# Kernel optimization log

Hardware: AMD Instinct MI355X
Metric: run time of the kernel (lower is better)

The kernel has to match this reference:

```python
import jax, jax.numpy as jnp
import numpy as np


def _register_translation(target_images, src_images, upsample_factor):
    # squeeze channel dim -> (B, H, W), promote to complex for FFT
    tgt = target_images[..., 0].astype(jnp.complex64)
    src = src_images[..., 0].astype(jnp.complex64)
    B, H, W = tgt.shape

    target_freq = jnp.fft.fft2(tgt)
    src_freq = jnp.fft.fft2(src)
    # cross-power spectrum (skimage register_translation convention)
    image_product = src_freq * jnp.conj(target_freq)
    cross_corr = jnp.fft.ifft2(image_product)

    # coarse (integer-pixel) peak
    abs_cc = jnp.abs(cross_corr).reshape(B, -1)
    idx = jnp.argmax(abs_cc, axis=1)
    maxima = jnp.stack([idx // W, idx % W], axis=1).astype(jnp.float32)  # (B,2)
    shape_f = jnp.array([H, W], jnp.float32)
    midpoints = jnp.array([H // 2, W // 2], jnp.float32)  # fix(axis_size/2)
    shifts = jnp.where(maxima > midpoints, maxima - shape_f, maxima)

    if upsample_factor > 1:
        uf = float(upsample_factor)
        shifts = jnp.round(shifts * uf) / uf
        region = int(np.ceil(upsample_factor * 1.5))  # upsampled region size
        dftshift = float(np.fix(region / 2.0))
        offsets = dftshift - shifts * uf  # (B,2) sample region offsets

        r_idx = jnp.arange(region, dtype=jnp.float32)
        freq_r = (jnp.fft.fftfreq(H) * H).astype(jnp.float32)  # ifftshift(arange(H)-H//2)
        freq_c = (jnp.fft.fftfreq(W) * W).astype(jnp.float32)
        two_pi = 2.0 * np.pi

        # per-batch small DFT kernels: row (B, region, H), col (B, W, region)
        row_ang = (two_pi / (H * uf)) * (r_idx[None, :, None] - offsets[:, 0][:, None, None]) * freq_r[None, None, :]
        col_ang = (two_pi / (W * uf)) * freq_c[None, :, None] * (r_idx[None, None, :] - offsets[:, 1][:, None, None])
        row_k = jnp.exp(-1j * row_ang)
        col_k = jnp.exp(-1j * col_ang)

        # upsampled DFT of conj(image_product), then conjugate back
        cc_up = jnp.conj(jnp.einsum('brh,bhw,bwc->brc', row_k, jnp.conj(image_product), col_k))
        abs_up = jnp.abs(cc_up).reshape(B, -1)
        idx2 = jnp.argmax(abs_up, axis=1)
        max2 = jnp.stack([idx2 // region, idx2 % region], axis=1).astype(jnp.float32) - dftshift
        shifts = shifts + max2 / uf

    return shifts  # (B, 2) -- (row_shift, col_shift)


def setup_inputs() -> dict:
    key = jax.random.key(0)
    k1, k2 = jax.random.split(key)
    B, H, W = 32, 512, 512
    target_images = jax.random.normal(k1, (B, H, W, 1), dtype=jnp.float32)
    src_images = jax.random.normal(k2, (B, H, W, 1), dtype=jnp.float32)
    return {"target_images": target_images, "src_images": src_images, "upsample_factor": 20}


def reference(target_images, src_images, upsample_factor):
    return _register_translation(target_images, src_images, upsample_factor)
```

## Files before the change

kernel.cpp:

```cpp
#include <hip/hip_runtime.h>
#include <math.h>

#define BN 32
#define HN 512
#define WN 512
#define REGION 30
#define RPAD 32
#define UFV 20.0f
#define DFTSHIFT 15.0f
#define TWO_PI 6.2831853071795864769f
#define HS 8
#define HCH (HN / HS)
#define WS 4

typedef float2 cplx;

__device__ __forceinline__ cplx cmul(cplx a, cplx b){
    return make_float2(a.x*b.x - a.y*b.y, a.x*b.y + a.y*b.x);
}
__device__ __forceinline__ cplx cadd(cplx a, cplx b){
    return make_float2(a.x + b.x, a.y + b.y);
}
__device__ __forceinline__ cplx csub(cplx a, cplx b){
    return make_float2(a.x - b.x, a.y - b.y);
}
__device__ __forceinline__ int brev6(int i){ return (int)(__brev((unsigned)i) >> 26); }
__device__ __forceinline__ int csl(int h, int c){ return c * 546 + h + (h >> 4); }

#define BFLY(a,b,w){ cplx t_ = cmul(w,b); b = make_float2(a.x - t_.x, a.y - t_.y); a = cadd(a, t_); }
#define BFLY1(a,b){ cplx t_ = b; b = make_float2(a.x - t_.x, a.y - t_.y); a = cadd(a, t_); }

__device__ __forceinline__ void fft512_regs(cplx* v, const float2* tw, cplx* ds, int lane){
    const cplx wI  = *(const cplx*)&tw[128];
    const cplx w8a = *(const cplx*)&tw[64];
    const cplx w8b = *(const cplx*)&tw[192];
    BFLY1(v[0],v[1]); BFLY1(v[2],v[3]); BFLY1(v[4],v[5]); BFLY1(v[6],v[7]);
    BFLY1(v[0],v[2]); BFLY(v[1],v[3],wI); BFLY1(v[4],v[6]); BFLY(v[5],v[7],wI);
    BFLY1(v[0],v[4]); BFLY(v[1],v[5],w8a); BFLY(v[2],v[6],wI); BFLY(v[3],v[7],w8b);
    const int h = lane >> 3, lo = lane & 7;
    const int bw = 9 * lane;
    const int br = 72 * h + lo;
    #pragma unroll
    for (int j = 0; j < 8; ++j) ds[bw + j] = v[j];
    asm volatile("s_waitcnt lgkmcnt(0)" ::: "memory");
    #pragma unroll
    for (int j = 0; j < 8; ++j) v[j] = ds[br + 9*j];
    {
        cplx wA = *(const cplx*)&tw[lo<<5];
        BFLY(v[0],v[1],wA); BFLY(v[2],v[3],wA); BFLY(v[4],v[5],wA); BFLY(v[6],v[7],wA);
        cplx wB0 = *(const cplx*)&tw[lo<<4], wB1 = *(const cplx*)&tw[128+(lo<<4)];
        BFLY(v[0],v[2],wB0); BFLY(v[1],v[3],wB1); BFLY(v[4],v[6],wB0); BFLY(v[5],v[7],wB1);
        cplx wC0 = *(const cplx*)&tw[lo<<3], wC1 = *(const cplx*)&tw[64+(lo<<3)];
        cplx wC2 = *(const cplx*)&tw[128+(lo<<3)], wC3 = *(const cplx*)&tw[192+(lo<<3)];
        BFLY(v[0],v[4],wC0); BFLY(v[1],v[5],wC1); BFLY(v[2],v[6],wC2); BFLY(v[3],v[7],wC3);
    }
    #pragma unroll
    for (int j = 0; j < 8; ++j) ds[br + 9*j] = v[j];
    asm volatile("s_waitcnt lgkmcnt(0)" ::: "memory");
    const int br3 = lane + (lane >> 3);
    #pragma unroll
    for (int j = 0; j < 8; ++j) v[j] = ds[br3 + 72*j];
    {
        cplx wD = *(const cplx*)&tw[lane<<2];
        BFLY(v[0],v[1],wD); BFLY(v[2],v[3],wD); BFLY(v[4],v[5],wD); BFLY(v[6],v[7],wD);
        cplx wE0 = *(const cplx*)&tw[lane<<1], wE1 = *(const cplx*)&tw[128+(lane<<1)];
        BFLY(v[0],v[2],wE0); BFLY(v[1],v[3],wE1); BFLY(v[4],v[6],wE0); BFLY(v[5],v[7],wE1);
        cplx wF0 = *(const cplx*)&tw[lane], wF1 = *(const cplx*)&tw[64+lane];
        cplx wF2 = *(const cplx*)&tw[128+lane], wF3 = *(const cplx*)&tw[192+lane];
        BFLY(v[0],v[4],wF0); BFLY(v[1],v[5],wF1); BFLY(v[2],v[6],wF2); BFLY(v[3],v[7],wF3);
    }
}

__global__ void __launch_bounds__(256) row_fft_pack(const float* __restrict__ tgt,
                                                    const float* __restrict__ src,
                                                    cplx* __restrict__ Fz){
    __shared__ float2 tw[256];
    __shared__ cplx ds[4 * 576];
    const int tid = threadIdx.x;
    { float sv, cv; sincosf(-TWO_PI * (float)tid * (1.0f/512.0f), &sv, &cv);
      tw[tid] = make_float2(cv, sv); }
    __syncthreads();
    const int wave = tid >> 6, lane = tid & 63;
    const int rid = blockIdx.x * 4 + wave;
    const float* tr = tgt + (size_t)rid * WN;
    const float* sr = src + (size_t)rid * WN;
    const int rb6 = brev6(lane);
    const int B3[8] = {0,256,128,384,64,320,192,448};
    cplx v[8];
    #pragma unroll
    for (int j = 0; j < 8; ++j){ int o = B3[j] + rb6; v[j] = make_float2(tr[o], sr[o]); }
    fft512_regs(v, (const float2*)tw, ds + wave * 576, lane);
    cplx* orow = Fz + (size_t)rid * WN;
    #pragma unroll
    for (int j = 0; j < 8; ++j) orow[64*j + lane] = v[j];
}

__device__ __forceinline__ void col_fft8(cplx* sm, const float2* tw, int tid){
    const cplx wI  = tw[128];
    const cplx w8a = tw[64];
    const cplx w8b = tw[192];
    const int c  = tid & 7;
    const int k0 = tid >> 3, k1 = k0 + 32;
    const int B3[8] = {0,256,128,384,64,320,192,448};
    cplx ya[8], yb[8];
    {
        const int r0 = brev6(k0), r1 = brev6(k1);
        #pragma unroll
        for (int m = 0; m < 8; ++m){
            ya[m] = sm[csl(B3[m] + r0, c)];
            yb[m] = sm[csl(B3[m] + r1, c)];
        }
    }
    __syncthreads();
    #define P0(x) \
        BFLY1(x[0],x[1]); BFLY1(x[2],x[3]); BFLY1(x[4],x[5]); BFLY1(x[6],x[7]); \
        BFLY1(x[0],x[2]); BFLY(x[1],x[3],wI); BFLY1(x[4],x[6]); BFLY(x[5],x[7],wI); \
        BFLY1(x[0],x[4]); BFLY(x[1],x[5],w8a); BFLY(x[2],x[6],wI); BFLY(x[3],x[7],w8b);
    P0(ya); P0(yb);
    #undef P0
    #pragma unroll
    for (int m = 0; m < 8; ++m){
        sm[csl(8*k0 + m, c)] = ya[m];
        sm[csl(8*k1 + m, c)] = yb[m];
    }
    __syncthreads();
    #pragma unroll
    for (int pass = 1; pass < 3; ++pass){
        const int st = 3*pass + 1;
        const int h1 = 1 << (st - 1);
        #pragma unroll
        for (int gi = 0; gi < 2; ++gi){
            const int k = (tid >> 3) + 32*gi;
            const int q = k & (h1 - 1);
            const int i0 = ((k >> (st - 1)) << (st + 2)) + q;
            cplx x[8];
            #pragma unroll
            for (int m = 0; m < 8; ++m) x[m] = sm[csl(i0 + m*h1, c)];
            cplx w1 = tw[q << (9 - st)];
            BFLY(x[0],x[1],w1); BFLY(x[2],x[3],w1); BFLY(x[4],x[5],w1); BFLY(x[6],x[7],w1);
            cplx w2a = tw[q << (8 - st)];
            cplx w2b = tw[(q << (8 - st)) + 128];
            BFLY(x[0],x[2],w2a); BFLY(x[1],x[3],w2b); BFLY(x[4],x[6],w2a); BFLY(x[5],x[7],w2b);
            cplx w30 = tw[q << (7 - st)];
            cplx w31 = tw[(q << (7 - st)) + 64];
            cplx w32 = tw[(q << (7 - st)) + 128];
            cplx w33 = tw[(q << (7 - st)) + 192];
            BFLY(x[0],x[4],w30); BFLY(x[1],x[5],w31); BFLY(x[2],x[6],w32); BFLY(x[3],x[7],w33);
            #pragma unroll
            for (int m = 0; m < 8; ++m) sm[csl(i0 + m*h1, c)] = x[m];
        }
        __syncthreads();
    }
}

__global__ void col_fft_fwd(cplx* __restrict__ buf){
    const int b  = blockIdx.y;
    const int w0 = blockIdx.x * 8;
    const int tid = threadIdx.x;
    __shared__ cplx sm[4368];
    __shared__ float2 tw[256];
    { float sv, cv; sincosf(-TWO_PI * (float)tid * (1.0f/512.0f), &sv, &cv);
      tw[tid] = make_float2(cv, sv); }
    cplx* base = buf + (size_t)b * HN * WN + w0;
    for (int idx = tid; idx < HN * 4; idx += 256){
        int h = idx >> 2, c2 = (idx & 3) << 1;
        float4 v = *(const float4*)(base + (size_t)h * WN + c2);
        sm[csl(h, c2)]     = make_float2(v.x, v.y);
        sm[csl(h, c2 + 1)] = make_float2(v.z, v.w);
    }
    __syncthreads();
    col_fft8(sm, (const float2*)tw, tid);
    for (int idx = tid; idx < HN * 4; idx += 256){
        int h = idx >> 2, c2 = (idx & 3) << 1;
        cplx a = sm[csl(h, c2)], d = sm[csl(h, c2 + 1)];
        *(float4*)(base + (size_t)h * WN + c2) = make_float4(a.x, a.y, d.x, d.y);
    }
}

__global__ void __launch_bounds__(256) cross_rowinv(cplx* __restrict__ Fz, cplx* __restrict__ cc){
    __shared__ float2 tw[256];
    __shared__ cplx ds[4 * 1184];
    const int tid = threadIdx.x;
    { float sv, cv; sincosf(TWO_PI * (float)tid * (1.0f/512.0f), &sv, &cv);
      tw[tid] = make_float2(cv, sv); }
    __syncthreads();
    const int wave = tid >> 6, lane = tid & 63;
    const int p = blockIdx.x * 4 + wave;
    if (p > 256) return;
    const int b = blockIdx.y;
    const int h1 = p, h2 = (HN - p) & (HN - 1);
    cplx* r1 = Fz + ((size_t)b * HN + h1) * WN;
    cplx* r2 = Fz + ((size_t)b * HN + h2) * WN;
    cplx* A = ds + wave * 1184;
    cplx* B = A + 592;
    #pragma unroll
    for (int u = 0; u < 8; ++u){
        A[lane + 64*u] = r1[lane + 64*u];
        B[lane + 64*u] = r2[lane + 64*u];
    }
    asm volatile("s_waitcnt lgkmcnt(0)" ::: "memory");
    const int rb6 = brev6(lane);
    const int B3[8] = {0,256,128,384,64,320,192,448};
    cplx v1[8];
    #pragma unroll
    for (int j = 0; j < 8; ++j){
        int w  = B3[j] + rb6;
        int wm = (WN - w) & (WN - 1);
        cplx Aw = A[w], Bw = B[w], Am = A[wm], Bm = B[wm];
        { cplx Bc = make_float2(Bm.x, -Bm.y);
          cplx s = cadd(Aw, Bc);
          cplx d = make_float2(Aw.x - Bc.x, Aw.y - Bc.y);
          cplx D = make_float2(d.x*s.x + d.y*s.y, d.y*s.x - d.x*s.y);
          v1[j] = make_float2(0.25f * D.y, -0.25f * D.x); }
        { cplx Ac = make_float2(Am.x, -Am.y);
          cplx s = cadd(Bw, Ac);
          cplx d = make_float2(Bw.x - Ac.x, Bw.y - Ac.y);
          cplx D = make_float2(d.x*s.x + d.y*s.y, d.y*s.x - d.x*s.y);
          r2[w] = make_float2(0.25f * D.y, -0.25f * D.x); }
        r1[w] = v1[j];
    }
    fft512_regs(v1, (const float2*)tw, A, lane);
    cplx* c1 = cc + ((size_t)b * HN + h1) * WN;
    #pragma unroll
    for (int j = 0; j < 8; ++j) c1[64*j + lane] = v1[j];
}

__global__ void colinv_argmax(const cplx* __restrict__ buf, float2* __restrict__ cand){
    const int b  = blockIdx.y;
    const int w0 = blockIdx.x * 8;
    const int tid = threadIdx.x;
    __shared__ cplx sm[4368];
    __shared__ float2 tw[256];
    { float sv, cv; sincosf(TWO_PI * (float)tid * (1.0f/512.0f), &sv, &cv);
      tw[tid] = make_float2(cv, sv); }
    const cplx* base = buf + (size_t)b * HN * WN + w0;
    for (int idx = tid; idx < 257 * 4; idx += 256){
        int h = idx >> 2, c2 = (idx & 3) << 1;
        float4 v = *(const float4*)(base + (size_t)h * WN + c2);
        sm[csl(h, c2)]     = make_float2(v.x, v.y);
        sm[csl(h, c2 + 1)] = make_float2(v.z, v.w);
    }
    __syncthreads();
    for (int idx = tid; idx < 255 * 8; idx += 256){
        int h = 257 + (idx >> 3), c = idx & 7;
        cplx v = sm[csl(HN - h, c)];
        sm[csl(h, c)] = make_float2(v.x, -v.y);
    }
    __syncthreads();
    col_fft8(sm, (const float2*)tw, tid);
    float best = -1.0f; int bidx = 0x7fffffff;
    for (int idx = tid; idx < HN * 8; idx += 256){
        int h = idx >> 3, c = idx & 7;
        cplx v = sm[csl(h, c)];
        float mm = v.x * v.x + v.y * v.y;
        if (mm > best){ best = mm; bidx = h * WN + w0 + c; }
    }
    __shared__ float vals[256];
    __shared__ int   idxs[256];
    vals[tid] = best; idxs[tid] = bidx;
    __syncthreads();
    for (int s = 128; s > 0; s >>= 1){
        if (tid < s){
            if (vals[tid + s] > vals[tid] ||
                (vals[tid + s] == vals[tid] && idxs[tid + s] < idxs[tid])){
                vals[tid] = vals[tid + s]; idxs[tid] = idxs[tid + s];
            }
        }
        __syncthreads();
    }
    if (tid == 0) cand[b * 64 + blockIdx.x] = make_float2(vals[0], __int_as_float(idxs[0]));
}

__global__ void coarse_reduce(const float2* __restrict__ cand, float* __restrict__ small){
    const int b = blockIdx.x, t = threadIdx.x;
    float2 c = cand[b * 64 + t];
    float v = c.x; int ix = __float_as_int(c.y);
    for (int off = 32; off > 0; off >>= 1){
        float v2 = __shfl_down(v, off);
        int   i2 = __shfl_down(ix, off);
        if (v2 > v || (v2 == v && i2 < ix)){ v = v2; ix = i2; }
    }
    if (t == 0){
        int row = ix / WN, col = ix % WN;
        float sr = (row > HN / 2) ? (float)(row - HN) : (float)row;
        float sc = (col > WN / 2) ? (float)(col - WN) : (float)col;
        small[b * 4 + 0] = sr;
        small[b * 4 + 1] = sc;
        small[b * 4 + 2] = DFTSHIFT - sr * UFV;
        small[b * 4 + 3] = DFTSHIFT - sc * UFV;
    }
}

__global__ void __launch_bounds__(256, 3) upsample_T(const cplx* __restrict__ P,
                                                     const float* __restrict__ small,
                                                     cplx* __restrict__ Tpart){
    const int b = blockIdx.y, hs = blockIdx.z;
    const int tid = threadIdx.x;
    const int wp = tid & 31;
    const int rbase = tid >> 5;
    const int w = blockIdx.x * 64 + wp * 2;
    const int h0 = hs * HCH;
    const float off0 = small[b * 4 + 2];
    const float CC = TWO_PI / (HN * UFV);
    __shared__ float2 rk[RPAD][HCH];
    for (int idx = tid; idx < RPAD * HCH; idx += 256){
        int r = idx >> 6, hh = idx & (HCH - 1);
        int h = h0 + hh;
        float fr = (h < HN / 2) ? (float)h : (float)(h - HN);
        float sv, cv; sincosf(-CC * ((float)r - off0) * fr, &sv, &cv);
        rk[r][hh] = make_float2(cv, sv);
    }
    __syncthreads();
    cplx a0[4], a1[4];
    #pragma unroll
    for (int u = 0; u < 4; ++u){ a0[u] = make_float2(0.f,0.f); a1[u] = make_float2(0.f,0.f); }
    const cplx* pc = P + ((size_t)b * HN + h0) * WN + w;

    float4 pvA[4], pvB[4];
    #pragma unroll
    for (int k = 0; k < 4; ++k) pvA[k] = *(const float4*)(pc + (size_t)k * WN);

    #pragma unroll 1
    for (int hh = 0; hh < HCH; hh += 8){
        #pragma unroll
        for (int k = 0; k < 4; ++k)
            pvB[k] = *(const float4*)(pc + (size_t)(hh + 4 + k) * WN);
        #pragma unroll
        for (int k = 0; k < 4; ++k){
            #pragma unroll
            for (int u = 0; u < 4; ++u){
                cplx wv = rk[rbase * 4 + u][hh + k];
                a0[u].x += wv.x * pvA[k].x + wv.y * pvA[k].y;
                a0[u].y += wv.y * pvA[k].x - wv.x * pvA[k].y;
                a1[u].x += wv.x * pvA[k].z + wv.y * pvA[k].w;
                a1[u].y += wv.y * pvA[k].z - wv.x * pvA[k].w;
            }
        }
        if (hh + 8 < HCH){
            #pragma unroll
            for (int k = 0; k < 4; ++k)
                pvA[k] = *(const float4*)(pc + (size_t)(hh + 8 + k) * WN);
        }
        #pragma unroll
        for (int k = 0; k < 4; ++k){
            #pragma unroll
            for (int u = 0; u < 4; ++u){
                cplx wv = rk[rbase * 4 + u][hh + 4 + k];
                a0[u].x += wv.x * pvB[k].x + wv.y * pvB[k].y;
                a0[u].y += wv.y * pvB[k].x - wv.x * pvB[k].y;
                a1[u].x += wv.x * pvB[k].z + wv.y * pvB[k].w;
                a1[u].y += wv.y * pvB[k].z - wv.x * pvB[k].w;
            }
        }
    }

    #pragma unroll
    for (int u = 0; u < 4; ++u){
        int r = rbase * 4 + u;
        if (r < REGION){
            float4* dst = (float4*)(Tpart + (((size_t)hs * BN + b) * REGION + r) * WN + w);
            *dst = make_float4(a0[u].x, a0[u].y, a1[u].x, a1[u].y);
        }
    }
}

__global__ void upsample_U_part(const cplx* __restrict__ Tpart, const cplx* __restrict__ P,
                                const float* __restrict__ small, cplx* __restrict__ Upart){
    const int ws = blockIdx.x, b = blockIdx.y;
    const int tid = threadIdx.x;
    const int w0 = ws * 64;
    const float off0 = small[b * 4 + 2];
    const float off1 = small[b * 4 + 3];
    const float CW = TWO_PI / (WN * UFV);
    const float CH = TWO_PI / (HN * UFV);
    __shared__ float2 Ts[REGION][64];
    __shared__ float2 ck[64][REGION];
    __shared__ float2 p256[64];
    __shared__ float2 T256s[REGION];
    const size_t TS = (size_t)BN * REGION * WN;
    for (int idx = tid; idx < REGION * 64; idx += 256){
        int r = idx >> 6, ww = idx & 63;
        cplx s = make_float2(0.f, 0.f);
        #pragma unroll
        for (int hs = 0; hs < HS; ++hs)
            s = cadd(s, Tpart[(size_t)hs * TS + ((size_t)b * REGION + r) * WN + w0 + ww]);
        Ts[r][ww] = s;
    }
    if (tid < 64) p256[tid] = P[((size_t)b * HN + 256) * WN + w0 + tid];
    if (ws == 0 && tid >= 64 && tid < 64 + REGION){
        int r = tid - 64;
        cplx s = make_float2(0.f, 0.f);
        #pragma unroll
        for (int hs = 0; hs < HS; ++hs)
            s = cadd(s, Tpart[(size_t)hs * TS + ((size_t)b * REGION + r) * WN + 256]);
        T256s[r] = s;
    }
    for (int idx = tid; idx < 64 * REGION; idx += 256){
        int ww = idx / REGION, c = idx - ww * REGION;
        int w = w0 + ww;
        float sv, cv; sincosf(-CW * (float)w * ((float)c - off1), &sv, &cv);
        ck[ww][c] = make_float2(cv, sv);
    }
    __syncthreads();
    const int start = (ws == 0) ? 1 : 0;
    #pragma unroll
    for (int q = 0; q < 4; ++q){
        int o = tid + 256 * q;
        if (o < REGION * REGION){
            int r = o / REGION, c = o - r * REGION;
            float racc = 0.f;
            cplx s2 = make_float2(0.f, 0.f);
            for (int ww = start; ww < 64; ++ww){
                float2 T = Ts[r][ww], K = ck[ww][c];
                racc += T.x * K.x - T.y * K.y;
                float2 pv = p256[ww];
                s2.x += pv.x * K.x + pv.y * K.y;
                s2.y += pv.y * K.x - pv.x * K.y;
            }
            float th = CH * ((float)r - off0) * 256.0f;
            float snt = sinf(th);
            cplx contrib = make_float2(2.f * racc - 2.f * snt * s2.y,
                                       2.f * snt * s2.x);
            if (ws == 0){
                contrib = cadd(contrib, Ts[r][0]);
                float s256, c256; sincosf(CW * 256.0f * ((float)c - off1), &s256, &c256);
                contrib = cadd(contrib, cmul(T256s[r], make_float2(c256, s256)));
            }
            Upart[((size_t)ws * BN + b) * (REGION * REGION) + o] = contrib;
        }
    }
}

__global__ void upsample_argmax(const cplx* __restrict__ Upart, const float* __restrict__ small,
                                float* __restrict__ out){
    const int b = blockIdx.x;
    const int tid = threadIdx.x;
    float best = -1.0f; int bidx = 0x7fffffff;
    #pragma unroll
    for (int q = 0; q < 4; ++q){
        int o = tid + 256 * q;
        if (o < REGION * REGION){
            cplx u = make_float2(0.f, 0.f);
            #pragma unroll
            for (int ws = 0; ws < WS; ++ws)
                u = cadd(u, Upart[((size_t)ws * BN + b) * (REGION * REGION) + o]);
            float m = u.x * u.x + u.y * u.y;
            if (m > best){ best = m; bidx = o; }
        }
    }
    __shared__ float vals[256];
    __shared__ int   idxs[256];
    vals[tid] = best; idxs[tid] = bidx;
    __syncthreads();
    for (int s = 128; s > 0; s >>= 1){
        if (tid < s){
            if (vals[tid + s] > vals[tid] ||
                (vals[tid + s] == vals[tid] && idxs[tid + s] < idxs[tid])){
                vals[tid] = vals[tid + s]; idxs[tid] = idxs[tid + s];
            }
        }
        __syncthreads();
    }
    if (tid == 0){
        int o = idxs[0];
        float r = (float)(o / REGION) - DFTSHIFT;
        float c = (float)(o % REGION) - DFTSHIFT;
        out[b * 2 + 0] = small[b * 4 + 0] + r / UFV;
        out[b * 2 + 1] = small[b * 4 + 1] + c / UFV;
    }
}

extern "C" void kernel_launch(void* const* d_in, const int* in_sizes, int n_in,
                              void* d_out, int out_size, void* d_ws, size_t ws_size,
                              hipStream_t stream){
    const float* tgt = (const float*)d_in[0];
    const float* src = (const float*)d_in[1];
    float* out = (float*)d_out;

    const size_t BIG = (size_t)BN * HN * WN;
    cplx* buf1 = (cplx*)d_ws;
    cplx* buf2 = buf1 + BIG;
    float* small = (float*)(buf2 + BIG);
    float2* cand = (float2*)(small + 128);

    const size_t TSTRIDE = (size_t)BN * REGION * WN;
    cplx* Tpart = buf2;
    cplx* Upart = buf2 + HS * TSTRIDE;

    dim3 blk(256);
    row_fft_pack<<<dim3(BN * HN / 4), blk, 0, stream>>>(tgt, src, buf1);
    col_fft_fwd<<<dim3(WN / 8, BN), blk, 0, stream>>>(buf1);
    cross_rowinv<<<dim3((257 + 3) / 4, BN), blk, 0, stream>>>(buf1, buf2);
    colinv_argmax<<<dim3(WN / 8, BN), blk, 0, stream>>>(buf2, cand);
    coarse_reduce<<<dim3(BN), dim3(64), 0, stream>>>(cand, small);
    upsample_T<<<dim3(5, BN, HS), blk, 0, stream>>>(buf1, small, Tpart);
    upsample_U_part<<<dim3(WS, BN), blk, 0, stream>>>(Tpart, buf1, small, Upart);
    upsample_argmax<<<dim3(BN), blk, 0, stream>>>(Upart, small, out);
}
```

Before: 182.3 us.

## Use 512-thread column FFT blocks with bit-reversed smem load and shuffle argmax

The column FFT kernels move from 256 to 512 threads per block, so each thread processes one radix-8 group per pass instead of two. The bit-reversal permutation is now applied while writing global data into shared memory, which removes the separate read-then-sync step of the first pass. The argmax block reduction switches from a shared-memory tree with many barriers to wave shuffles plus a small cross-wave combine. The aim is more parallelism per column tile and fewer barriers, at the cost of higher register and thread demand per block, which may lower the number of resident blocks.

```diff
diff --git a/kernel.cpp b/kernel.cpp
--- a/kernel.cpp
+++ b/kernel.cpp
@@ -24,6 +24,7 @@
 __device__ __forceinline__ cplx csub(cplx a, cplx b){
     return make_float2(a.x - b.x, a.y - b.y);
 }
+__device__ __forceinline__ int brev9(int i){ return (int)(__brev((unsigned)i) >> 23); }
 __device__ __forceinline__ int brev6(int i){ return (int)(__brev((unsigned)i) >> 26); }
 __device__ __forceinline__ int csl(int h, int c){ return c * 546 + h + (h >> 4); }
 
@@ -95,82 +96,67 @@
     for (int j = 0; j < 8; ++j) orow[64*j + lane] = v[j];
 }
 
-__device__ __forceinline__ void col_fft8(cplx* sm, const float2* tw, int tid){
+__device__ __forceinline__ void col_fft8_t512(cplx* sm, const float2* tw, int tid){
     const cplx wI  = tw[128];
     const cplx w8a = tw[64];
     const cplx w8b = tw[192];
-    const int c  = tid & 7;
-    const int k0 = tid >> 3, k1 = k0 + 32;
-    const int B3[8] = {0,256,128,384,64,320,192,448};
-    cplx ya[8], yb[8];
+    const int c = tid & 7;
+    const int k = tid >> 3;
     {
-        const int r0 = brev6(k0), r1 = brev6(k1);
-        #pragma unroll
-        for (int m = 0; m < 8; ++m){
-            ya[m] = sm[csl(B3[m] + r0, c)];
-            yb[m] = sm[csl(B3[m] + r1, c)];
-        }
-    }
-    __syncthreads();
-    #define P0(x) \
-        BFLY1(x[0],x[1]); BFLY1(x[2],x[3]); BFLY1(x[4],x[5]); BFLY1(x[6],x[7]); \
-        BFLY1(x[0],x[2]); BFLY(x[1],x[3],wI); BFLY1(x[4],x[6]); BFLY(x[5],x[7],wI); \
-        BFLY1(x[0],x[4]); BFLY(x[1],x[5],w8a); BFLY(x[2],x[6],wI); BFLY(x[3],x[7],w8b);
-    P0(ya); P0(yb);
-    #undef P0
-    #pragma unroll
-    for (int m = 0; m < 8; ++m){
-        sm[csl(8*k0 + m, c)] = ya[m];
-        sm[csl(8*k1 + m, c)] = yb[m];
+        cplx y[8];
+        #pragma unroll
+        for (int m = 0; m < 8; ++m) y[m] = sm[csl(8*k + m, c)];
+        BFLY1(y[0],y[1]); BFLY1(y[2],y[3]); BFLY1(y[4],y[5]); BFLY1(y[6],y[7]);
+        BFLY1(y[0],y[2]); BFLY(y[1],y[3],wI); BFLY1(y[4],y[6]); BFLY(y[5],y[7],wI);
+        BFLY1(y[0],y[4]); BFLY(y[1],y[5],w8a); BFLY(y[2],y[6],wI); BFLY(y[3],y[7],w8b);
+        #pragma unroll
+        for (int m = 0; m < 8; ++m) sm[csl(8*k + m, c)] = y[m];
     }
     __syncthreads();
     #pragma unroll
     for (int pass = 1; pass < 3; ++pass){
         const int st = 3*pass + 1;
         const int h1 = 1 << (st - 1);
-        #pragma unroll
-        for (int gi = 0; gi < 2; ++gi){
-            const int k = (tid >> 3) + 32*gi;
-            const int q = k & (h1 - 1);
-            const int i0 = ((k >> (st - 1)) << (st + 2)) + q;
-            cplx x[8];
-            #pragma unroll
-            for (int m = 0; m < 8; ++m) x[m] = sm[csl(i0 + m*h1, c)];
-            cplx w1 = tw[q << (9 - st)];
-            BFLY(x[0],x[1],w1); BFLY(x[2],x[3],w1); BFLY(x[4],x[5],w1); BFLY(x[6],x[7],w1);
-            cplx w2a = tw[q << (8 - st)];
-            cplx w2b = tw[(q << (8 - st)) + 128];
-            BFLY(x[0],x[2],w2a); BFLY(x[1],x[3],w2b); BFLY(x[4],x[6],w2a); BFLY(x[5],x[7],w2b);
-            cplx w30 = tw[q << (7 - st)];
-            cplx w31 = tw[(q << (7 - st)) + 64];
-            cplx w32 = tw[(q << (7 - st)) + 128];
-            cplx w33 = tw[(q << (7 - st)) + 192];
-            BFLY(x[0],x[4],w30); BFLY(x[1],x[5],w31); BFLY(x[2],x[6],w32); BFLY(x[3],x[7],w33);
-            #pragma unroll
-            for (int m = 0; m < 8; ++m) sm[csl(i0 + m*h1, c)] = x[m];
-        }
+        const int q = k & (h1 - 1);
+        const int i0 = ((k >> (st - 1)) << (st + 2)) + q;
+        cplx x[8];
+        #pragma unroll
+        for (int m = 0; m < 8; ++m) x[m] = sm[csl(i0 + m*h1, c)];
+        cplx w1 = tw[q << (9 - st)];
+        BFLY(x[0],x[1],w1); BFLY(x[2],x[3],w1); BFLY(x[4],x[5],w1); BFLY(x[6],x[7],w1);
+        cplx w2a = tw[q << (8 - st)];
+        cplx w2b = tw[(q << (8 - st)) + 128];
+        BFLY(x[0],x[2],w2a); BFLY(x[1],x[3],w2b); BFLY(x[4],x[6],w2a); BFLY(x[5],x[7],w2b);
+        cplx w30 = tw[q << (7 - st)];
+        cplx w31 = tw[(q << (7 - st)) + 64];
+        cplx w32 = tw[(q << (7 - st)) + 128];
+        cplx w33 = tw[(q << (7 - st)) + 192];
+        BFLY(x[0],x[4],w30); BFLY(x[1],x[5],w31); BFLY(x[2],x[6],w32); BFLY(x[3],x[7],w33);
+        #pragma unroll
+        for (int m = 0; m < 8; ++m) sm[csl(i0 + m*h1, c)] = x[m];
         __syncthreads();
     }
 }
 
-__global__ void col_fft_fwd(cplx* __restrict__ buf){
+__global__ void __launch_bounds__(512) col_fft_fwd(cplx* __restrict__ buf){
     const int b  = blockIdx.y;
     const int w0 = blockIdx.x * 8;
     const int tid = threadIdx.x;
     __shared__ cplx sm[4368];
     __shared__ float2 tw[256];
-    { float sv, cv; sincosf(-TWO_PI * (float)tid * (1.0f/512.0f), &sv, &cv);
+    if (tid < 256){ float sv, cv; sincosf(-TWO_PI * (float)tid * (1.0f/512.0f), &sv, &cv);
       tw[tid] = make_float2(cv, sv); }
     cplx* base = buf + (size_t)b * HN * WN + w0;
-    for (int idx = tid; idx < HN * 4; idx += 256){
+    for (int idx = tid; idx < HN * 4; idx += 512){
         int h = idx >> 2, c2 = (idx & 3) << 1;
         float4 v = *(const float4*)(base + (size_t)h * WN + c2);
-        sm[csl(h, c2)]     = make_float2(v.x, v.y);
-        sm[csl(h, c2 + 1)] = make_float2(v.z, v.w);
-    }
-    __syncthreads();
-    col_fft8(sm, (const float2*)tw, tid);
-    for (int idx = tid; idx < HN * 4; idx += 256){
+        int hb = brev9(h);
+        sm[csl(hb, c2)]     = make_float2(v.x, v.y);
+        sm[csl(hb, c2 + 1)] = make_float2(v.z, v.w);
+    }
+    __syncthreads();
+    col_fft8_t512(sm, (const float2*)tw, tid);
+    for (int idx = tid; idx < HN * 4; idx += 512){
         int h = idx >> 2, c2 = (idx & 3) << 1;
         cplx a = sm[csl(h, c2)], d = sm[csl(h, c2 + 1)];
         *(float4*)(base + (size_t)h * WN + c2) = make_float4(a.x, a.y, d.x, d.y);
@@ -225,50 +211,55 @@
     for (int j = 0; j < 8; ++j) c1[64*j + lane] = v1[j];
 }
 
-__global__ void colinv_argmax(const cplx* __restrict__ buf, float2* __restrict__ cand){
+__global__ void __launch_bounds__(512) colinv_argmax(const cplx* __restrict__ buf,
+                                                     float2* __restrict__ cand){
     const int b  = blockIdx.y;
     const int w0 = blockIdx.x * 8;
     const int tid = threadIdx.x;
     __shared__ cplx sm[4368];
     __shared__ float2 tw[256];
-    { float sv, cv; sincosf(TWO_PI * (float)tid * (1.0f/512.0f), &sv, &cv);
+    __shared__ float wv_[8];
+    __shared__ int   wi_[8];
+    if (tid < 256){ float sv, cv; sincosf(TWO_PI * (float)tid * (1.0f/512.0f), &sv, &cv);
       tw[tid] = make_float2(cv, sv); }
     const cplx* base = buf + (size_t)b * HN * WN + w0;
-    for (int idx = tid; idx < 257 * 4; idx += 256){
+    for (int idx = tid; idx < 257 * 4; idx += 512){
         int h = idx >> 2, c2 = (idx & 3) << 1;
         float4 v = *(const float4*)(base + (size_t)h * WN + c2);
-        sm[csl(h, c2)]     = make_float2(v.x, v.y);
-        sm[csl(h, c2 + 1)] = make_float2(v.z, v.w);
-    }
-    __syncthreads();
-    for (int idx = tid; idx < 255 * 8; idx += 256){
+        int hb = brev9(h);
+        sm[csl(hb, c2)]     = make_float2(v.x, v.y);
+        sm[csl(hb, c2 + 1)] = make_float2(v.z, v.w);
+    }
+    __syncthreads();
+    for (int idx = tid; idx < 255 * 8; idx += 512){
         int h = 257 + (idx >> 3), c = idx & 7;
-        cplx v = sm[csl(HN - h, c)];
-        sm[csl(h, c)] = make_float2(v.x, -v.y);
-    }
-    __syncthreads();
-    col_fft8(sm, (const float2*)tw, tid);
+        cplx v = sm[csl(brev9(HN - h), c)];
+        sm[csl(brev9(h), c)] = make_float2(v.x, -v.y);
+    }
+    __syncthreads();
+    col_fft8_t512(sm, (const float2*)tw, tid);
     float best = -1.0f; int bidx = 0x7fffffff;
-    for (int idx = tid; idx < HN * 8; idx += 256){
+    for (int idx = tid; idx < HN * 8; idx += 512){
         int h = idx >> 3, c = idx & 7;
         cplx v = sm[csl(h, c)];
         float mm = v.x * v.x + v.y * v.y;
         if (mm > best){ best = mm; bidx = h * WN + w0 + c; }
     }
-    __shared__ float vals[256];
-    __shared__ int   idxs[256];
-    vals[tid] = best; idxs[tid] = bidx;
-    __syncthreads();
-    for (int s = 128; s > 0; s >>= 1){
-        if (tid < s){
-            if (vals[tid + s] > vals[tid] ||
-                (vals[tid + s] == vals[tid] && idxs[tid + s] < idxs[tid])){
-                vals[tid] = vals[tid + s]; idxs[tid] = idxs[tid + s];
-            }
-        }
-        __syncthreads();
-    }
-    if (tid == 0) cand[b * 64 + blockIdx.x] = make_float2(vals[0], __int_as_float(idxs[0]));
+    for (int off = 32; off > 0; off >>= 1){
+        float v2 = __shfl_down(best, off);
+        int   i2 = __shfl_down(bidx, off);
+        if (v2 > best || (v2 == best && i2 < bidx)){ best = v2; bidx = i2; }
+    }
+    if ((tid & 63) == 0){ wv_[tid >> 6] = best; wi_[tid >> 6] = bidx; }
+    __syncthreads();
+    if (tid == 0){
+        float bv = wv_[0]; int bx = wi_[0];
+        #pragma unroll
+        for (int w2 = 1; w2 < 8; ++w2){
+            if (wv_[w2] > bv || (wv_[w2] == bv && wi_[w2] < bx)){ bv = wv_[w2]; bx = wi_[w2]; }
+        }
+        cand[b * 64 + blockIdx.x] = make_float2(bv, __int_as_float(bx));
+    }
 }
 
 __global__ void coarse_reduce(const float2* __restrict__ cand, float* __restrict__ small){
@@ -489,9 +480,9 @@
 
     dim3 blk(256);
     row_fft_pack<<<dim3(BN * HN / 4), blk, 0, stream>>>(tgt, src, buf1);
-    col_fft_fwd<<<dim3(WN / 8, BN), blk, 0, stream>>>(buf1);
+    col_fft_fwd<<<dim3(WN / 8, BN), dim3(512), 0, stream>>>(buf1);
     cross_rowinv<<<dim3((257 + 3) / 4, BN), blk, 0, stream>>>(buf1, buf2);
-    colinv_argmax<<<dim3(WN / 8, BN), blk, 0, stream>>>(buf2, cand);
+    colinv_argmax<<<dim3(WN / 8, BN), dim3(512), 0, stream>>>(buf2, cand);
     coarse_reduce<<<dim3(BN), dim3(64), 0, stream>>>(cand, small);
     upsample_T<<<dim3(5, BN, HS), blk, 0, stream>>>(buf1, small, Tpart);
     upsample_U_part<<<dim3(WS, BN), blk, 0, stream>>>(Tpart, buf1, small, Upart);
```

Result: no change. 183.2 us (+0.5%).
